# Kernel optimization log

Measured on AMD Instinct MI355X. Metric: run time of the kernel, lower is better.

The kernel has to match this reference:

```python
import math
import jax, jax.numpy as jnp
import numpy as np

DMODEL = 512
NUM_HEADS = 8
HEAD_DIM = DMODEL // NUM_HEADS
MAX_LEN = 1024
L = 2 * MAX_LEN - 1  # 2047
B = 4
S = 1024  # src_len == max_len


def setup_inputs() -> dict:
    key = jax.random.key(0)
    ks = jax.random.split(key, 12)
    f32 = jnp.float32
    inp = {
        "query": jax.random.normal(ks[0], (B, S, DMODEL), f32),
        "key": jax.random.normal(ks[1], (B, S, DMODEL), f32),
        "value": jax.random.normal(ks[2], (B, S, DMODEL), f32),
        # nn.Linear weights (y = x @ W.T + b)
        "Wq": jax.random.normal(ks[3], (DMODEL, DMODEL), f32) * 0.02,
        "bq": jnp.zeros((DMODEL,), f32),
        "Wk": jax.random.normal(ks[4], (DMODEL, DMODEL), f32) * 0.02,
        "bk": jnp.zeros((DMODEL,), f32),
        "Wv": jax.random.normal(ks[5], (DMODEL, DMODEL), f32) * 0.02,
        "bv": jnp.zeros((DMODEL,), f32),
        # relative position tables (torch.randn init)
        "quaver_Er": jax.random.normal(ks[6], (NUM_HEADS, L, HEAD_DIM), f32),
        "beat_Er": jax.random.normal(ks[7], (NUM_HEADS, L // 4, HEAD_DIM), f32),
        "bar_Er": jax.random.normal(ks[8], (NUM_HEADS, L // 16, HEAD_DIM), f32),
    }
    return inp


def _skew(QEr):
    # QEr: [b, h, S, 2S-1] -> [b, h, S, S] via pad-reshape-slice trick
    b, h, s, l = QEr.shape
    x = jnp.pad(QEr, ((0, 0), (0, 0), (0, 0), (0, 1)))        # [b,h,S,2S]
    x = x.reshape(b, h, -1)                                    # [b,h,S*2S]
    x = jnp.pad(x, ((0, 0), (0, 0), (0, l - s)))               # [b,h,(S+1)*(2S-1)]
    x = x.reshape(b, h, s + 1, l)
    return x[:, :, :s, -s:]


def _skew_chunked(QEr, rep):
    # Faithful to skew_beat/skew_bar: repeat_interleave(rep) along last dim, then
    # roll each chunk of `rep` rows (chunk i) by i*rep, then take last S cols.
    b, h, s, lr = QEr.shape
    x = jnp.repeat(QEr, rep, axis=-1)                          # [b,h,S,rep*lr]
    w = rep * lr
    shifts = (jnp.arange(s) // rep) * rep                      # [S]
    # torch.roll: out[c] = in[(c - shift) mod W]
    cols = (jnp.arange(w)[None, :] - shifts[:, None]) % w      # [S, W]
    x = jnp.take_along_axis(x, cols[None, None], axis=-1)
    return x[:, :, :s, -s:]


def reference(query, key, value, Wq, bq, Wk, bk, Wv, bv, quaver_Er, beat_Er, bar_Er):
    bs, src_len, d_model = query.shape
    h, hd = NUM_HEADS, HEAD_DIM
    max_len = MAX_LEN

    q = (query @ Wq.T + bq).reshape(bs, src_len, h, hd).transpose(0, 2, 1, 3)   # [b,h,S,d]
    k = (key @ Wk.T + bk).reshape(bs, src_len, h, hd).transpose(0, 2, 3, 1)      # [b,h,d,S]
    v = (value @ Wv.T + bv).reshape(bs, src_len, h, hd).transpose(0, 2, 1, 3)    # [b,h,S,d]

    Er_q = quaver_Er[:, max_len - src_len:max_len + src_len, :]                  # [h,2S-1,d]
    Er_b = beat_Er[:, (max_len - src_len) // 4:(max_len + src_len) // 4, :]      # [h,~S/2,d]
    Er_r = bar_Er[:, (max_len - src_len) // 16:(max_len + src_len) // 16, :]     # [h,~S/8,d]

    QEr_q = jnp.einsum('bhsd,hld->bhsl', q, Er_q)
    QEr_b = jnp.einsum('bhsd,hld->bhsl', q, Er_b)
    QEr_r = jnp.einsum('bhsd,hld->bhsl', q, Er_r)

    Srel = _skew(QEr_q)
    Srel_beat = _skew_chunked(QEr_b, 4)
    Srel_bar = _skew_chunked(QEr_r, 16)

    attn = (jnp.matmul(q, k) + Srel + Srel_beat + Srel_bar) / math.sqrt(hd)
    attn = jax.nn.softmax(attn, axis=-1)
    out = jnp.matmul(attn, v)                                                    # [b,h,S,d]
    out = out.transpose(0, 2, 1, 3).reshape(bs, src_len, d_model)
    return out, attn
```

## Files before the change

### kernel.cpp

```cpp
#include <hip/hip_runtime.h>


typedef float f32x4 __attribute__((ext_vector_type(4)));
typedef short s16x8 __attribute__((ext_vector_type(8)));
typedef short s16x4 __attribute__((ext_vector_type(4)));
typedef __bf16 bf16x8 __attribute__((ext_vector_type(8)));

static __device__ __forceinline__ short f2bf(float f) {
    return __builtin_bit_cast(short, (__bf16)f);
}
static __device__ __forceinline__ float bf2f(short s) {
    union { unsigned u; float f; } v;
    v.u = ((unsigned)(unsigned short)s) << 16;
    return v.f;
}
static __device__ __forceinline__ f32x4 MM(s16x8 a, s16x8 b, f32x4 c) {
    return __builtin_amdgcn_mfma_f32_16x16x32_bf16(
        __builtin_bit_cast(bf16x8, a), __builtin_bit_cast(bf16x8, b), c, 0, 0, 0);
}

struct CvtArgs {
    const float* src[9];
    short* dst[9];
    unsigned n[9];
};

__global__ __launch_bounds__(256) void convert_kernel(CvtArgs a) {
    const int ai = blockIdx.y;
    const unsigned n = a.n[ai];
    const float* __restrict__ s = a.src[ai];
    short* __restrict__ d = a.dst[ai];
    const unsigned stride = gridDim.x * 256 * 8;
    for (unsigned base = (blockIdx.x * 256 + threadIdx.x) * 8; base < n; base += stride) {
        f32x4 v0 = *(const f32x4*)(s + base);
        f32x4 v1 = *(const f32x4*)(s + base + 4);
        s16x8 o;
        o[0] = f2bf(v0[0]); o[1] = f2bf(v0[1]); o[2] = f2bf(v0[2]); o[3] = f2bf(v0[3]);
        o[4] = f2bf(v1[0]); o[5] = f2bf(v1[1]); o[6] = f2bf(v1[2]); o[7] = f2bf(v1[3]);
        *(s16x8*)(d + base) = o;
    }
}

__global__ __launch_bounds__(256, 2) void proj_kernel(
    const short* __restrict__ queryb, const short* __restrict__ keyb, const short* __restrict__ valueb,
    const short* __restrict__ Wqb, const float* __restrict__ bq,
    const short* __restrict__ Wkb, const float* __restrict__ bk,
    const short* __restrict__ Wvb, const float* __restrict__ bv,
    short* __restrict__ qb, short* __restrict__ kb, short* __restrict__ vT)
{
    const int tid = threadIdx.x;
    const int wid = tid >> 6, lane = tid & 63;
    const int l15 = lane & 15, grp = lane >> 4;
    const int gid = blockIdx.x * 4 + wid;
    const int z = gid >> 11;
    const int r = gid & 2047;

    const short *Am, *Bm;
    const float* bias;
    int a0, b0;
    if (z == 0)      { Am = queryb; Bm = Wqb;    bias = bq; a0 = (r >> 4) * 32; b0 = (r & 15) * 32; }
    else if (z == 1) { Am = keyb;   Bm = Wkb;    bias = bk; a0 = (r >> 4) * 32; b0 = (r & 15) * 32; }
    else             { Am = Wvb;    Bm = valueb; bias = bv; a0 = (r >> 7) * 32; b0 = (r & 127) * 32; }

    f32x4 acc[2][2];
    #pragma unroll
    for (int i = 0; i < 2; ++i)
        #pragma unroll
        for (int j = 0; j < 2; ++j)
            acc[i][j] = f32x4{0.f, 0.f, 0.f, 0.f};

    const short* arow0 = Am + (size_t)(a0 + l15) * 512 + grp * 8;
    const short* brow0 = Bm + (size_t)(b0 + l15) * 512 + grp * 8;

    s16x8 aA[2], bA[2], aB[2], bB[2], aC[2], bC[2];
    #pragma unroll
    for (int i = 0; i < 2; ++i) {
        aA[i] = *(const s16x8*)(arow0 + (size_t)i * 16 * 512);
        bA[i] = *(const s16x8*)(brow0 + (size_t)i * 16 * 512);
        aB[i] = *(const s16x8*)(arow0 + (size_t)i * 16 * 512 + 32);
        bB[i] = *(const s16x8*)(brow0 + (size_t)i * 16 * 512 + 32);
        aC[i] = *(const s16x8*)(arow0 + (size_t)i * 16 * 512 + 64);
        bC[i] = *(const s16x8*)(brow0 + (size_t)i * 16 * 512 + 64);
    }
    for (int kk = 0; kk < 512; kk += 32) {
        #pragma unroll
        for (int i = 0; i < 2; ++i)
            #pragma unroll
            for (int j = 0; j < 2; ++j)
                acc[i][j] = MM(aA[i], bA[j], acc[i][j]);
        #pragma unroll
        for (int i = 0; i < 2; ++i) { aA[i] = aB[i]; bA[i] = bB[i]; aB[i] = aC[i]; bB[i] = bC[i]; }
        const int kn = kk + 96;
        if (kn < 512) {
            #pragma unroll
            for (int i = 0; i < 2; ++i) {
                aC[i] = *(const s16x8*)(arow0 + (size_t)i * 16 * 512 + kn);
                bC[i] = *(const s16x8*)(brow0 + (size_t)i * 16 * 512 + kn);
            }
        }
    }

    if (z < 2) {
        short* dst = (z == 0) ? qb : kb;
        #pragma unroll
        for (int j = 0; j < 2; ++j) {
            const int n = b0 + j * 16 + l15;
            const float bval = bias[n];
            const int h = n >> 6, d = n & 63;
            #pragma unroll
            for (int i = 0; i < 2; ++i)
                #pragma unroll
                for (int g = 0; g < 4; ++g) {
                    const int m = a0 + i * 16 + grp * 4 + g;
                    const int bb = m >> 10, s = m & 1023;
                    dst[(size_t)((bb * 8 + h) * 1024 + s) * 64 + d] = f2bf(acc[i][j][g] + bval);
                }
        }
    } else {
        #pragma unroll
        for (int i = 0; i < 2; ++i)
            #pragma unroll
            for (int g = 0; g < 4; ++g) {
                const int n = a0 + i * 16 + grp * 4 + g;
                const float bval = bias[n];
                const int h = n >> 6, d = n & 63;
                #pragma unroll
                for (int j = 0; j < 2; ++j) {
                    const int m = b0 + j * 16 + l15;
                    const int bb = m >> 10, s = m & 1023;
                    vT[(size_t)((bb * 8 + h) * 64 + d) * 1024 + s] = f2bf(acc[i][j][g] + bval);
                }
            }
    }
}

__global__ __launch_bounds__(512, 2) void attn_kernel(
    const short* __restrict__ Eqb, const short* __restrict__ Ebb, const short* __restrict__ Errb,
    const short* __restrict__ qb, const short* __restrict__ kb, const short* __restrict__ vT,
    float* __restrict__ out, float* __restrict__ attn)
{
    __shared__ __align__(16) char smem[119104];
    float* RSUM = (float*)(smem + 110400);
    float* PACC = (float*)(smem + 110912);
    const int PSS = 1032;

    const int tid = threadIdx.x;
    const int wid = tid >> 6, lane = tid & 63;
    const int l15 = lane & 15, grp = lane >> 4;

    const int orig = blockIdx.x;
    const int bid = (orig & 7) * 32 + (orig >> 3);

    const int bh = bid >> 3;
    const int chunk = bid & 7;
    const int h = bh & 7;
    const int b = bh >> 3;

    const short* EqH = Eqb  + (size_t)h * 2047 * 64;
    const short* EbH = Ebb  + (size_t)h * 511 * 64;
    const short* ErH = Errb + (size_t)h * 127 * 64;
    const short* qbH = qb + (size_t)bh * 1024 * 64;
    const short* kbH = kb + (size_t)bh * 1024 * 64;
    const short* vTH = vT + (size_t)bh * 64 * 1024;

    auto buildT = [&](int i0s, int bb01, s16x8 q0, s16x8 q1) {
        short* RQD = (short*)(smem + bb01 * 42240);
        short* RBT = (short*)(smem + 84480 + bb01 * 10400);
        short* RRT = (short*)(smem + 105280 + bb01 * 2560);
        const int qbase = 1008 - i0s;
        for (int cs = wid; cs < 65; cs += 8) {
            int erow = qbase + cs * 16 + l15; if (erow > 2046) erow = 2046;
            const short* ep = EqH + (size_t)erow * 64 + grp * 8;
            s16x8 e0 = *(const s16x8*)ep;
            s16x8 e1 = *(const s16x8*)(ep + 32);
            f32x4 a = f32x4{0.f, 0.f, 0.f, 0.f};
            a = MM(q0, e0, a);
            a = MM(q1, e1, a);
            const int cb0 = cs * 16 + l15;
            #pragma unroll
            for (int g = 0; g < 4; ++g) {
                const int ii = grp * 4 + g;
                RQD[(cb0 + ii) * 20 + ii] = f2bf(a[g]);
            }
        }
        const int bbase = 252 - (i0s >> 2);
        for (int cs = wid; cs < 17; cs += 8) {
            int erow = bbase + cs * 16 + l15; if (erow > 510) erow = 510;
            const short* ep = EbH + (size_t)erow * 64 + grp * 8;
            s16x8 e0 = *(const s16x8*)ep;
            s16x8 e1 = *(const s16x8*)(ep + 32);
            f32x4 a = f32x4{0.f, 0.f, 0.f, 0.f};
            a = MM(q0, e0, a);
            a = MM(q1, e1, a);
            const int c = cs * 16 + l15;
            if (c < 260) {
                #pragma unroll
                for (int g = 0; g < 4; ++g)
                    RBT[c * 20 + grp * 4 + g] = f2bf(a[g]);
            }
        }
        const int rbase = 63 - (i0s >> 4);
        if (wid < 4) {
            const int erow = rbase + wid * 16 + l15;
            const short* ep = ErH + (size_t)erow * 64 + grp * 8;
            s16x8 e0 = *(const s16x8*)ep;
            s16x8 e1 = *(const s16x8*)(ep + 32);
            f32x4 a = f32x4{0.f, 0.f, 0.f, 0.f};
            a = MM(q0, e0, a);
            a = MM(q1, e1, a);
            #pragma unroll
            for (int g = 0; g < 4; ++g)
                RRT[(wid * 16 + l15) * 20 + grp * 4 + g] = f2bf(a[g]);
        }
    };

    const int i0_0 = chunk * 128;
    s16x8 qA0 = *(const s16x8*)(qbH + (size_t)(i0_0 + l15) * 64 + grp * 8);
    s16x8 qA1 = *(const s16x8*)(qbH + (size_t)(i0_0 + l15) * 64 + 32 + grp * 8);

    s16x8 kf[8][2];
    #pragma unroll
    for (int t = 0; t < 8; ++t) {
        const short* kp = kbH + (size_t)(wid * 128 + t * 16 + l15) * 64 + grp * 8;
        kf[t][0] = *(const s16x8*)kp;
        kf[t][1] = *(const s16x8*)(kp + 32);
    }
    const int cv = wid >> 1, kh = wid & 1;
    const short* vrow = vTH + (size_t)(cv * 16 + l15) * 1024 + kh * 512 + grp * 8;
    s16x8 vreg[16];
    #pragma unroll
    for (int kk = 0; kk < 16; ++kk)
        vreg[kk] = *(const s16x8*)(vrow + kk * 32);

    buildT(i0_0, 0, qA0, qA1);
    __syncthreads();

    const float SC = 0.125f * 1.4426950408889634f;

    #pragma unroll 2
    for (int s = 0; s < 8; ++s) {
        const int cur = s & 1;
        const int i0 = chunk * 128 + s * 16;
        short* RQDc = (short*)(smem + cur * 42240);
        short* RBTc = (short*)(smem + 84480 + cur * 10400);
        short* RRTc = (short*)(smem + 105280 + cur * 2560);
        short* PS   = (short*)(smem + cur * 42240);

        f32x4 p[8];
        #pragma unroll
        for (int t = 0; t < 8; ++t) {
            const int jb = wid * 128 + t * 16;
            const int j = jb + l15;
            f32x4 a = f32x4{0.f, 0.f, 0.f, 0.f};
            a = MM(qA0, kf[t][0], a);
            a = MM(qA1, kf[t][1], a);
            const int cb = (j >> 2) + 3 - grp;
            const int cr = wid * 8 + t;
            s16x4 gq4 = *(const s16x4*)&RQDc[(j + 15) * 20 + grp * 4];
            s16x4 rb4 = *(const s16x4*)&RBTc[cb * 20 + grp * 4];
            s16x4 rr4 = *(const s16x4*)&RRTc[cr * 20 + grp * 4];
            f32x4 pe;
            #pragma unroll
            for (int g = 0; g < 4; ++g)
                pe[g] = exp2f((a[g] + bf2f(gq4[g]) + bf2f(rb4[g]) + bf2f(rr4[g])) * SC);
            p[t] = pe;
        }

        s16x8 qn0, qn1;
        if (s < 7) {
            qn0 = *(const s16x8*)(qbH + (size_t)(i0 + 16 + l15) * 64 + grp * 8);
            qn1 = *(const s16x8*)(qbH + (size_t)(i0 + 16 + l15) * 64 + 32 + grp * 8);
        }

        f32x4 rs = p[0];
        #pragma unroll
        for (int t = 1; t < 8; ++t) rs += p[t];
        #pragma unroll
        for (int m = 1; m < 16; m <<= 1)
            #pragma unroll
            for (int g = 0; g < 4; ++g)
                rs[g] += __shfl_xor(rs[g], m, 64);
        if (l15 == 0) {
            #pragma unroll
            for (int g = 0; g < 4; ++g)
                RSUM[(grp * 4 + g) * 8 + wid] = rs[g];
        }
        __syncthreads();

        float rinv[4];
        #pragma unroll
        for (int g = 0; g < 4; ++g) {
            f32x4 s0 = *(const f32x4*)&RSUM[(grp * 4 + g) * 8];
            f32x4 s1 = *(const f32x4*)&RSUM[(grp * 4 + g) * 8 + 4];
            rinv[g] = 1.0f / (s0[0] + s0[1] + s0[2] + s0[3] + s1[0] + s1[1] + s1[2] + s1[3]);
        }

        if (s < 7) buildT(i0 + 16, cur ^ 1, qn0, qn1);

        #pragma unroll
        for (int t = 0; t < 8; ++t) {
            const int jb = wid * 128 + t * 16;
            #pragma unroll
            for (int g = 0; g < 4; ++g)
                PS[(grp * 4 + g) * PSS + jb + l15] = f2bf(p[t][g] * rinv[g]);
        }
        __syncthreads();

        {
            float* abase = attn + (size_t)(bh * 1024 + i0) * 1024;
            #pragma unroll
            for (int rr = 0; rr < 2; ++rr) {
                const int row = wid * 2 + rr;
                float* arow = abase + (size_t)row * 1024;
                #pragma unroll
                for (int pass = 0; pass < 4; ++pass) {
                    const int col = pass * 256 + lane * 4;
                    s16x4 v4 = *(const s16x4*)&PS[row * PSS + col];
                    f32x4 o;
                    o[0] = bf2f(v4[0]); o[1] = bf2f(v4[1]);
                    o[2] = bf2f(v4[2]); o[3] = bf2f(v4[3]);
                    *(f32x4*)(arow + col) = o;
                }
            }
        }
        {
            f32x4 acc = f32x4{0.f, 0.f, 0.f, 0.f};
            const short* prow = PS + (size_t)l15 * PSS + kh * 512 + grp * 8;
            #pragma unroll
            for (int kk = 0; kk < 16; ++kk) {
                s16x8 af = *(const s16x8*)(prow + kk * 32);
                acc = MM(af, vreg[kk], acc);
            }
            #pragma unroll
            for (int g = 0; g < 4; ++g)
                PACC[(wid * 16 + grp * 4 + g) * 16 + l15] = acc[g];
        }
        __syncthreads();

        if (wid < 4) {
            #pragma unroll
            for (int g = 0; g < 4; ++g) {
                const int row = grp * 4 + g;
                const float v = PACC[((2 * wid) * 16 + row) * 16 + l15]
                              + PACC[((2 * wid + 1) * 16 + row) * 16 + l15];
                out[(size_t)(b * 1024 + i0 + row) * 512 + h * 64 + wid * 16 + l15] = v;
            }
        }

        if (s < 7) { qA0 = qn0; qA1 = qn1; }
    }
}

extern "C" void kernel_launch(void* const* d_in, const int* in_sizes, int n_in,
                              void* d_out, int out_size, void* d_ws, size_t ws_size,
                              hipStream_t stream)
{
    const float* query = (const float*)d_in[0];
    const float* key   = (const float*)d_in[1];
    const float* value = (const float*)d_in[2];
    const float* Wq = (const float*)d_in[3];
    const float* bq = (const float*)d_in[4];
    const float* Wk = (const float*)d_in[5];
    const float* bk = (const float*)d_in[6];
    const float* Wv = (const float*)d_in[7];
    const float* bv = (const float*)d_in[8];
    const float* Eq = (const float*)d_in[9];
    const float* Eb = (const float*)d_in[10];
    const float* Er = (const float*)d_in[11];

    float* out  = (float*)d_out;
    float* attn = out + (size_t)4 * 1024 * 512;

    short* qb     = (short*)d_ws;
    short* kb     = qb     + 2097152;
    short* vT     = kb     + 2097152;
    short* queryb = vT     + 2097152;
    short* keyb   = queryb + 2097152;
    short* valueb = keyb   + 2097152;
    short* Wqb    = valueb + 2097152;
    short* Wkb    = Wqb    + 262144;
    short* Wvb    = Wkb    + 262144;
    short* Eqb    = Wvb    + 262144;
    short* Ebb    = Eqb    + 1048064;
    short* Errb   = Ebb    + 261632;

    CvtArgs a;
    a.src[0] = query; a.dst[0] = queryb; a.n[0] = 2097152;
    a.src[1] = key;   a.dst[1] = keyb;   a.n[1] = 2097152;
    a.src[2] = value; a.dst[2] = valueb; a.n[2] = 2097152;
    a.src[3] = Wq;    a.dst[3] = Wqb;    a.n[3] = 262144;
    a.src[4] = Wk;    a.dst[4] = Wkb;    a.n[4] = 262144;
    a.src[5] = Wv;    a.dst[5] = Wvb;    a.n[5] = 262144;
    a.src[6] = Eq;    a.dst[6] = Eqb;    a.n[6] = 1048064;
    a.src[7] = Eb;    a.dst[7] = Ebb;    a.n[7] = 261632;
    a.src[8] = Er;    a.dst[8] = Errb;   a.n[8] = 65024;

    convert_kernel<<<dim3(256, 9), 256, 0, stream>>>(a);
    proj_kernel<<<1536, 256, 0, stream>>>(queryb, keyb, valueb,
                                          Wqb, bq, Wkb, bk, Wvb, bv, qb, kb, vT);
    attn_kernel<<<256, 512, 0, stream>>>(Eqb, Ebb, Errb, qb, kb, vT, out, attn);
}
```

Baseline: 159.3 us.

## Transpose score MFMA, restructure skew tables, enlarge projection tiles, normalize PV after

The projection kernel now uses 64x64 tiles per wave with 128-thread blocks, swaps operand roles, and writes vectorized bias-added outputs. The attention kernel computes scores transposed (K as A operand), so each lane holds four consecutive columns. The relative-position tables are stored in row-major skewed layouts, probabilities are written unnormalized to a swizzled LDS buffer, and PV normalization is deferred to the reduction. attn is written directly from registers in fp32 instead of round-tripping through bf16 LDS, and the convert grid is enlarged. This removes a sync and the bf16 requantization of attn, at the cost of more LDS (about 155 KB, which likely drops occupancy to one block per CU).

After: 129.5 us. 1.23x faster.

```diff
diff --git a/kernel.cpp b/kernel.cpp
--- a/kernel.cpp
+++ b/kernel.cpp
@@ -18,6 +18,7 @@
     return __builtin_amdgcn_mfma_f32_16x16x32_bf16(
         __builtin_bit_cast(bf16x8, a), __builtin_bit_cast(bf16x8, b), c, 0, 0, 0);
 }
+#define KEEP(x) asm volatile("" : "+v"(x))
 
 struct CvtArgs {
     const float* src[9];
@@ -41,7 +42,7 @@
     }
 }
 
-__global__ __launch_bounds__(256, 2) void proj_kernel(
+__global__ __launch_bounds__(128, 2) void proj_kernel(
     const short* __restrict__ queryb, const short* __restrict__ keyb, const short* __restrict__ valueb,
     const short* __restrict__ Wqb, const float* __restrict__ bq,
     const short* __restrict__ Wkb, const float* __restrict__ bk,
@@ -51,86 +52,86 @@
     const int tid = threadIdx.x;
     const int wid = tid >> 6, lane = tid & 63;
     const int l15 = lane & 15, grp = lane >> 4;
-    const int gid = blockIdx.x * 4 + wid;
-    const int z = gid >> 11;
-    const int r = gid & 2047;
+    const int gid = blockIdx.x * 2 + wid;
+    const int z = gid >> 9;
+    const int r = gid & 511;
 
     const short *Am, *Bm;
     const float* bias;
     int a0, b0;
-    if (z == 0)      { Am = queryb; Bm = Wqb;    bias = bq; a0 = (r >> 4) * 32; b0 = (r & 15) * 32; }
-    else if (z == 1) { Am = keyb;   Bm = Wkb;    bias = bk; a0 = (r >> 4) * 32; b0 = (r & 15) * 32; }
-    else             { Am = Wvb;    Bm = valueb; bias = bv; a0 = (r >> 7) * 32; b0 = (r & 127) * 32; }
-
-    f32x4 acc[2][2];
+    if (z == 0)      { Am = Wqb;    Bm = queryb; bias = bq; a0 = (r >> 6) * 64; b0 = (r & 63) * 64; }
+    else if (z == 1) { Am = Wkb;    Bm = keyb;   bias = bk; a0 = (r >> 6) * 64; b0 = (r & 63) * 64; }
+    else             { Am = valueb; Bm = Wvb;    bias = bv; a0 = (r >> 3) * 64; b0 = (r & 7) * 64; }
+
+    f32x4 acc[4][4];
     #pragma unroll
-    for (int i = 0; i < 2; ++i)
-        #pragma unroll
-        for (int j = 0; j < 2; ++j)
+    for (int i = 0; i < 4; ++i)
+        #pragma unroll
+        for (int j = 0; j < 4; ++j)
             acc[i][j] = f32x4{0.f, 0.f, 0.f, 0.f};
 
     const short* arow0 = Am + (size_t)(a0 + l15) * 512 + grp * 8;
     const short* brow0 = Bm + (size_t)(b0 + l15) * 512 + grp * 8;
 
-    s16x8 aA[2], bA[2], aB[2], bB[2], aC[2], bC[2];
+    s16x8 aA[4], bA[4], aB[4], bB[4];
     #pragma unroll
-    for (int i = 0; i < 2; ++i) {
+    for (int i = 0; i < 4; ++i) {
         aA[i] = *(const s16x8*)(arow0 + (size_t)i * 16 * 512);
         bA[i] = *(const s16x8*)(brow0 + (size_t)i * 16 * 512);
-        aB[i] = *(const s16x8*)(arow0 + (size_t)i * 16 * 512 + 32);
-        bB[i] = *(const s16x8*)(brow0 + (size_t)i * 16 * 512 + 32);
-        aC[i] = *(const s16x8*)(arow0 + (size_t)i * 16 * 512 + 64);
-        bC[i] = *(const s16x8*)(brow0 + (size_t)i * 16 * 512 + 64);
     }
     for (int kk = 0; kk < 512; kk += 32) {
-        #pragma unroll
-        for (int i = 0; i < 2; ++i)
-            #pragma unroll
-            for (int j = 0; j < 2; ++j)
+        const int kn = kk + 32;
+        if (kn < 512) {
+            #pragma unroll
+            for (int i = 0; i < 4; ++i) {
+                aB[i] = *(const s16x8*)(arow0 + (size_t)i * 16 * 512 + kn);
+                bB[i] = *(const s16x8*)(brow0 + (size_t)i * 16 * 512 + kn);
+            }
+        }
+        #pragma unroll
+        for (int i = 0; i < 4; ++i)
+            #pragma unroll
+            for (int j = 0; j < 4; ++j)
                 acc[i][j] = MM(aA[i], bA[j], acc[i][j]);
         #pragma unroll
-        for (int i = 0; i < 2; ++i) { aA[i] = aB[i]; bA[i] = bB[i]; aB[i] = aC[i]; bB[i] = bC[i]; }
-        const int kn = kk + 96;
-        if (kn < 512) {
-            #pragma unroll
-            for (int i = 0; i < 2; ++i) {
-                aC[i] = *(const s16x8*)(arow0 + (size_t)i * 16 * 512 + kn);
-                bC[i] = *(const s16x8*)(brow0 + (size_t)i * 16 * 512 + kn);
-            }
-        }
+        for (int i = 0; i < 4; ++i) { aA[i] = aB[i]; bA[i] = bB[i]; }
     }
 
     if (z < 2) {
         short* dst = (z == 0) ? qb : kb;
         #pragma unroll
-        for (int j = 0; j < 2; ++j) {
+        for (int i = 0; i < 4; ++i) {
+            const int f0 = a0 + i * 16 + grp * 4;
+            const f32x4 bv4 = *(const f32x4*)&bias[f0];
+            const int h = f0 >> 6, d0 = f0 & 63;
+            #pragma unroll
+            for (int j = 0; j < 4; ++j) {
+                const int srow = b0 + j * 16 + l15;
+                const int bb = srow >> 10, sl = srow & 1023;
+                s16x4 o;
+                #pragma unroll
+                for (int g = 0; g < 4; ++g)
+                    o[g] = f2bf(acc[i][j][g] + bv4[g]);
+                *(s16x4*)&dst[(size_t)((bb * 8 + h) * 1024 + sl) * 64 + d0] = o;
+            }
+        }
+    } else {
+        #pragma unroll
+        for (int j = 0; j < 4; ++j) {
             const int n = b0 + j * 16 + l15;
             const float bval = bias[n];
             const int h = n >> 6, d = n & 63;
             #pragma unroll
-            for (int i = 0; i < 2; ++i)
+            for (int i = 0; i < 4; ++i) {
+                const int s0 = a0 + i * 16 + grp * 4;
+                const int bb = s0 >> 10, sl = s0 & 1023;
+                s16x4 o;
                 #pragma unroll
-                for (int g = 0; g < 4; ++g) {
-                    const int m = a0 + i * 16 + grp * 4 + g;
-                    const int bb = m >> 10, s = m & 1023;
-                    dst[(size_t)((bb * 8 + h) * 1024 + s) * 64 + d] = f2bf(acc[i][j][g] + bval);
-                }
-        }
-    } else {
-        #pragma unroll
-        for (int i = 0; i < 2; ++i)
-            #pragma unroll
-            for (int g = 0; g < 4; ++g) {
-                const int n = a0 + i * 16 + grp * 4 + g;
-                const float bval = bias[n];
-                const int h = n >> 6, d = n & 63;
-                #pragma unroll
-                for (int j = 0; j < 2; ++j) {
-                    const int m = b0 + j * 16 + l15;
-                    const int bb = m >> 10, s = m & 1023;
-                    vT[(size_t)((bb * 8 + h) * 64 + d) * 1024 + s] = f2bf(acc[i][j][g] + bval);
-                }
-            }
+                for (int g = 0; g < 4; ++g)
+                    o[g] = f2bf(acc[i][j][g] + bval);
+                *(s16x4*)&vT[(size_t)((bb * 8 + h) * 64 + d) * 1024 + sl] = o;
+            }
+        }
     }
 }
 
@@ -139,10 +140,9 @@
     const short* __restrict__ qb, const short* __restrict__ kb, const short* __restrict__ vT,
     float* __restrict__ out, float* __restrict__ attn)
 {
-    __shared__ __align__(16) char smem[119104];
-    float* RSUM = (float*)(smem + 110400);
-    float* PACC = (float*)(smem + 110912);
-    const int PSS = 1032;
+    __shared__ __align__(16) char smem[155008];
+    short* PS   = (short*)(smem + 86784);
+    float* PACC = (float*)(smem + 119680);
 
     const int tid = threadIdx.x;
     const int wid = tid >> 6, lane = tid & 63;
@@ -164,45 +164,47 @@
     const short* vTH = vT + (size_t)bh * 64 * 1024;
 
     auto buildT = [&](int i0s, int bb01, s16x8 q0, s16x8 q1) {
-        short* RQD = (short*)(smem + bb01 * 42240);
-        short* RBT = (short*)(smem + 84480 + bb01 * 10400);
-        short* RRT = (short*)(smem + 105280 + bb01 * 2560);
+        short* RQ2 = (short*)(smem + bb01 * 32896);
+        short* RB2 = (short*)(smem + 65792 + bb01 * 8320);
+        short* RR2 = (short*)(smem + 82432 + bb01 * 2176);
         const int qbase = 1008 - i0s;
         for (int cs = wid; cs < 65; cs += 8) {
-            int erow = qbase + cs * 16 + l15; if (erow > 2046) erow = 2046;
+            const int c = cs * 16 + l15;
+            int erow = qbase + c; if (erow > 2046) erow = 2046;
             const short* ep = EqH + (size_t)erow * 64 + grp * 8;
             s16x8 e0 = *(const s16x8*)ep;
             s16x8 e1 = *(const s16x8*)(ep + 32);
             f32x4 a = f32x4{0.f, 0.f, 0.f, 0.f};
             a = MM(q0, e0, a);
             a = MM(q1, e1, a);
-            const int cb0 = cs * 16 + l15;
             #pragma unroll
             for (int g = 0; g < 4; ++g) {
                 const int ii = grp * 4 + g;
-                RQD[(cb0 + ii) * 20 + ii] = f2bf(a[g]);
+                const int j = c - 15 + ii;
+                if (j >= 0 && j < 1024) RQ2[ii * 1028 + j] = f2bf(a[g]);
             }
         }
         const int bbase = 252 - (i0s >> 2);
         for (int cs = wid; cs < 17; cs += 8) {
-            int erow = bbase + cs * 16 + l15; if (erow > 510) erow = 510;
+            const int c = cs * 16 + l15;
+            int erow = bbase + c; if (erow > 510) erow = 510;
             const short* ep = EbH + (size_t)erow * 64 + grp * 8;
             s16x8 e0 = *(const s16x8*)ep;
             s16x8 e1 = *(const s16x8*)(ep + 32);
             f32x4 a = f32x4{0.f, 0.f, 0.f, 0.f};
             a = MM(q0, e0, a);
             a = MM(q1, e1, a);
-            const int c = cs * 16 + l15;
-            if (c < 260) {
+            const int jq = c - 3 + grp;
+            if (jq >= 0 && jq < 256) {
                 #pragma unroll
                 for (int g = 0; g < 4; ++g)
-                    RBT[c * 20 + grp * 4 + g] = f2bf(a[g]);
+                    RB2[(grp * 4 + g) * 260 + jq] = f2bf(a[g]);
             }
         }
         const int rbase = 63 - (i0s >> 4);
         if (wid < 4) {
-            const int erow = rbase + wid * 16 + l15;
-            const short* ep = ErH + (size_t)erow * 64 + grp * 8;
+            const int c = wid * 16 + l15;
+            const short* ep = ErH + (size_t)(rbase + c) * 64 + grp * 8;
             s16x8 e0 = *(const s16x8*)ep;
             s16x8 e1 = *(const s16x8*)(ep + 32);
             f32x4 a = f32x4{0.f, 0.f, 0.f, 0.f};
@@ -210,13 +212,13 @@
             a = MM(q1, e1, a);
             #pragma unroll
             for (int g = 0; g < 4; ++g)
-                RRT[(wid * 16 + l15) * 20 + grp * 4 + g] = f2bf(a[g]);
+                RR2[(grp * 4 + g) * 68 + c] = f2bf(a[g]);
         }
     };
 
-    const int i0_0 = chunk * 128;
-    s16x8 qA0 = *(const s16x8*)(qbH + (size_t)(i0_0 + l15) * 64 + grp * 8);
-    s16x8 qA1 = *(const s16x8*)(qbH + (size_t)(i0_0 + l15) * 64 + 32 + grp * 8);
+    const int i00 = chunk * 128;
+    s16x8 qA0 = *(const s16x8*)(qbH + (size_t)(i00 + l15) * 64 + grp * 8);
+    s16x8 qA1 = *(const s16x8*)(qbH + (size_t)(i00 + l15) * 64 + 32 + grp * 8);
 
     s16x8 kf[8][2];
     #pragma unroll
@@ -225,46 +227,32 @@
         kf[t][0] = *(const s16x8*)kp;
         kf[t][1] = *(const s16x8*)(kp + 32);
     }
-    const int cv = wid >> 1, kh = wid & 1;
-    const short* vrow = vTH + (size_t)(cv * 16 + l15) * 1024 + kh * 512 + grp * 8;
     s16x8 vreg[16];
     #pragma unroll
-    for (int kk = 0; kk < 16; ++kk)
-        vreg[kk] = *(const s16x8*)(vrow + kk * 32);
-
-    buildT(i0_0, 0, qA0, qA1);
+    for (int dvt = 0; dvt < 4; ++dvt)
+        #pragma unroll
+        for (int kc = 0; kc < 4; ++kc)
+            vreg[dvt * 4 + kc] = *(const s16x8*)(vTH + (size_t)(dvt * 16 + l15) * 1024
+                                                 + wid * 128 + kc * 32 + grp * 8);
+
+    buildT(i00, 0, qA0, qA1);
     __syncthreads();
 
     const float SC = 0.125f * 1.4426950408889634f;
-
-    #pragma unroll 2
+    const int swz = (l15 & 3) << 5;
+
     for (int s = 0; s < 8; ++s) {
+        #pragma unroll
+        for (int t = 0; t < 8; ++t) { KEEP(kf[t][0]); KEEP(kf[t][1]); }
+        #pragma unroll
+        for (int z = 0; z < 16; ++z) KEEP(vreg[z]);
+
         const int cur = s & 1;
         const int i0 = chunk * 128 + s * 16;
-        short* RQDc = (short*)(smem + cur * 42240);
-        short* RBTc = (short*)(smem + 84480 + cur * 10400);
-        short* RRTc = (short*)(smem + 105280 + cur * 2560);
-        short* PS   = (short*)(smem + cur * 42240);
-
-        f32x4 p[8];
-        #pragma unroll
-        for (int t = 0; t < 8; ++t) {
-            const int jb = wid * 128 + t * 16;
-            const int j = jb + l15;
-            f32x4 a = f32x4{0.f, 0.f, 0.f, 0.f};
-            a = MM(qA0, kf[t][0], a);
-            a = MM(qA1, kf[t][1], a);
-            const int cb = (j >> 2) + 3 - grp;
-            const int cr = wid * 8 + t;
-            s16x4 gq4 = *(const s16x4*)&RQDc[(j + 15) * 20 + grp * 4];
-            s16x4 rb4 = *(const s16x4*)&RBTc[cb * 20 + grp * 4];
-            s16x4 rr4 = *(const s16x4*)&RRTc[cr * 20 + grp * 4];
-            f32x4 pe;
-            #pragma unroll
-            for (int g = 0; g < 4; ++g)
-                pe[g] = exp2f((a[g] + bf2f(gq4[g]) + bf2f(rb4[g]) + bf2f(rr4[g])) * SC);
-            p[t] = pe;
-        }
+        short* RQ2c = (short*)(smem + cur * 32896);
+        short* RB2c = (short*)(smem + 65792 + cur * 8320);
+        short* RR2c = (short*)(smem + 82432 + cur * 2176);
+        float* RSUMc = (float*)(smem + 154496 + cur * 256);
 
         s16x8 qn0, qn1;
         if (s < 7) {
@@ -272,78 +260,88 @@
             qn1 = *(const s16x8*)(qbH + (size_t)(i0 + 16 + l15) * 64 + 32 + grp * 8);
         }
 
-        f32x4 rs = p[0];
-        #pragma unroll
-        for (int t = 1; t < 8; ++t) rs += p[t];
-        #pragma unroll
-        for (int m = 1; m < 16; m <<= 1)
+        f32x4 p[8];
+        #pragma unroll
+        for (int t = 0; t < 8; ++t) {
+            f32x4 a = f32x4{0.f, 0.f, 0.f, 0.f};
+            a = MM(kf[t][0], qA0, a);
+            a = MM(kf[t][1], qA1, a);
+            const int jb2 = wid * 128 + t * 16 + grp * 4;
+            s16x4 gq4 = *(const s16x4*)&RQ2c[l15 * 1028 + jb2];
+            const float rb = bf2f(RB2c[l15 * 260 + wid * 32 + t * 4 + grp]);
+            const float rr = bf2f(RR2c[l15 * 68 + wid * 8 + t]);
+            const float add = rb + rr;
+            f32x4 pe;
             #pragma unroll
             for (int g = 0; g < 4; ++g)
-                rs[g] += __shfl_xor(rs[g], m, 64);
-        if (l15 == 0) {
+                pe[g] = exp2f((a[g] + bf2f(gq4[g]) + add) * SC);
+            p[t] = pe;
+        }
+
+        float part = 0.f;
+        #pragma unroll
+        for (int t = 0; t < 8; ++t)
             #pragma unroll
             for (int g = 0; g < 4; ++g)
-                RSUM[(grp * 4 + g) * 8 + wid] = rs[g];
+                part += p[t][g];
+        part += __shfl_xor(part, 16, 64);
+        part += __shfl_xor(part, 32, 64);
+        if (lane < 16) RSUMc[lane * 8 + wid] = part;
+
+        #pragma unroll
+        for (int t = 0; t < 8; ++t) {
+            const int col = (wid * 128 + t * 16 + grp * 4) ^ swz;
+            s16x4 o;
+            #pragma unroll
+            for (int g = 0; g < 4; ++g) o[g] = f2bf(p[t][g]);
+            *(s16x4*)&PS[l15 * 1028 + col] = o;
         }
         __syncthreads();
 
-        float rinv[4];
-        #pragma unroll
-        for (int g = 0; g < 4; ++g) {
-            f32x4 s0 = *(const f32x4*)&RSUM[(grp * 4 + g) * 8];
-            f32x4 s1 = *(const f32x4*)&RSUM[(grp * 4 + g) * 8 + 4];
-            rinv[g] = 1.0f / (s0[0] + s0[1] + s0[2] + s0[3] + s1[0] + s1[1] + s1[2] + s1[3]);
+        float rinv;
+        {
+            f32x4 s0 = *(const f32x4*)&RSUMc[l15 * 8];
+            f32x4 s1 = *(const f32x4*)&RSUMc[l15 * 8 + 4];
+            rinv = 1.0f / (s0[0] + s0[1] + s0[2] + s0[3] + s1[0] + s1[1] + s1[2] + s1[3]);
         }
 
         if (s < 7) buildT(i0 + 16, cur ^ 1, qn0, qn1);
 
-        #pragma unroll
-        for (int t = 0; t < 8; ++t) {
-            const int jb = wid * 128 + t * 16;
-            #pragma unroll
-            for (int g = 0; g < 4; ++g)
-                PS[(grp * 4 + g) * PSS + jb + l15] = f2bf(p[t][g] * rinv[g]);
-        }
+        f32x4 acc[4];
+        #pragma unroll
+        for (int dvt = 0; dvt < 4; ++dvt) acc[dvt] = f32x4{0.f, 0.f, 0.f, 0.f};
+        #pragma unroll
+        for (int kc = 0; kc < 4; ++kc) {
+            const int col = (wid * 128 + kc * 32 + grp * 8) ^ swz;
+            s16x8 bfrag = *(const s16x8*)&PS[l15 * 1028 + col];
+            #pragma unroll
+            for (int dvt = 0; dvt < 4; ++dvt)
+                acc[dvt] = MM(vreg[dvt * 4 + kc], bfrag, acc[dvt]);
+        }
+        #pragma unroll
+        for (int dvt = 0; dvt < 4; ++dvt)
+            *(f32x4*)&PACC[(wid * 16 + l15) * 68 + dvt * 16 + grp * 4] = acc[dvt];
         __syncthreads();
 
+        if (tid < 256) {
+            const int i = tid >> 4, dvq = tid & 15;
+            f32x4 o = f32x4{0.f, 0.f, 0.f, 0.f};
+            #pragma unroll
+            for (int w = 0; w < 8; ++w)
+                o += *(const f32x4*)&PACC[(w * 16 + i) * 68 + dvq * 4];
+            f32x4 s0 = *(const f32x4*)&RSUMc[i * 8];
+            f32x4 s1 = *(const f32x4*)&RSUMc[i * 8 + 4];
+            const float ri = 1.0f / (s0[0] + s0[1] + s0[2] + s0[3] + s1[0] + s1[1] + s1[2] + s1[3]);
+            o *= ri;
+            *(f32x4*)&out[(size_t)(b * 1024 + i0 + i) * 512 + h * 64 + dvq * 4] = o;
+        }
+
         {
-            float* abase = attn + (size_t)(bh * 1024 + i0) * 1024;
-            #pragma unroll
-            for (int rr = 0; rr < 2; ++rr) {
-                const int row = wid * 2 + rr;
-                float* arow = abase + (size_t)row * 1024;
-                #pragma unroll
-                for (int pass = 0; pass < 4; ++pass) {
-                    const int col = pass * 256 + lane * 4;
-                    s16x4 v4 = *(const s16x4*)&PS[row * PSS + col];
-                    f32x4 o;
-                    o[0] = bf2f(v4[0]); o[1] = bf2f(v4[1]);
-                    o[2] = bf2f(v4[2]); o[3] = bf2f(v4[3]);
-                    *(f32x4*)(arow + col) = o;
-                }
-            }
-        }
-        {
-            f32x4 acc = f32x4{0.f, 0.f, 0.f, 0.f};
-            const short* prow = PS + (size_t)l15 * PSS + kh * 512 + grp * 8;
-            #pragma unroll
-            for (int kk = 0; kk < 16; ++kk) {
-                s16x8 af = *(const s16x8*)(prow + kk * 32);
-                acc = MM(af, vreg[kk], acc);
-            }
-            #pragma unroll
-            for (int g = 0; g < 4; ++g)
-                PACC[(wid * 16 + grp * 4 + g) * 16 + l15] = acc[g];
-        }
-        __syncthreads();
-
-        if (wid < 4) {
-            #pragma unroll
-            for (int g = 0; g < 4; ++g) {
-                const int row = grp * 4 + g;
-                const float v = PACC[((2 * wid) * 16 + row) * 16 + l15]
-                              + PACC[((2 * wid + 1) * 16 + row) * 16 + l15];
-                out[(size_t)(b * 1024 + i0 + row) * 512 + h * 64 + wid * 16 + l15] = v;
+            float* arow = attn + (size_t)(bh * 1024 + i0 + l15) * 1024;
+            #pragma unroll
+            for (int t = 0; t < 8; ++t) {
+                f32x4 o = p[t] * rinv;
+                *(f32x4*)&arow[wid * 128 + t * 16 + grp * 4] = o;
             }
         }
 
@@ -395,8 +393,8 @@
     a.src[7] = Eb;    a.dst[7] = Ebb;    a.n[7] = 261632;
     a.src[8] = Er;    a.dst[8] = Errb;   a.n[8] = 65024;
 
-    convert_kernel<<<dim3(256, 9), 256, 0, stream>>>(a);
-    proj_kernel<<<1536, 256, 0, stream>>>(queryb, keyb, valueb,
-                                          Wqb, bq, Wkb, bk, Wvb, bv, qb, kb, vT);
+    convert_kernel<<<dim3(1024, 9), 256, 0, stream>>>(a);
+    proj_kernel<<<768, 128, 0, stream>>>(queryb, keyb, valueb,
+                                         Wqb, bq, Wkb, bk, Wvb, bv, qb, kb, vT);
     attn_kernel<<<256, 512, 0, stream>>>(Eqb, Ebb, Errb, qb, kb, vT, out, attn);
 }
```
